# Performance work log

Hardware: AMD Instinct MI355X
Metric: run time of the kernel (lower is better)

The kernel has to match this reference:

```python
import jax, jax.numpy as jnp
import numpy as np

D = 10       # window length (days)
STRIDE = 10  # window stride


def setup_inputs() -> dict:
    key = jax.random.key(0)
    X = jax.random.normal(key, (16384, 15, 100), dtype=jnp.float32)
    return {"X": X}


def reference(X):
    # X: [B, n, T]
    B, n, T = X.shape
    w = (T - D) // STRIDE + 1
    # Gather all windows at once: [B, n, w, D]
    idx = jnp.arange(w)[:, None] * STRIDE + jnp.arange(D)[None, :]  # [w, D]
    win = X[:, :, idx]  # [B, n, w, D]

    mean = jnp.mean(win, axis=-1, keepdims=True)
    c = win - mean                                  # centered, [B, n, w, D]
    # torch.std is unbiased (ddof=1)
    std = jnp.sqrt(jnp.sum(c * c, axis=-1) / (D - 1))  # [B, n, w]

    # Population covariance between all channel pairs via one batched Gram matmul
    gram = jnp.einsum('biwd,bjwd->bijw', c, c) / D   # [B, n, n, w]

    # Pair order in the original: j=0..n-2 paired with k=j+1..n-1 == row-major upper triangle
    ii, jj = jnp.triu_indices(n, k=1)
    cov = gram[:, ii, jj]                            # [B, h, w]
    corr = cov / (std[:, ii] * std[:, jj])           # [B, h, w]
    return corr
```

## Files before the change

kernel.cpp:

```cpp
#include <hip/hip_runtime.h>


#define NB    16384
#define NSER  15
#define TLEN  100
#define DWIN  10
#define WCNT  10
#define NPAIR 105

__global__ __launch_bounds__(64, 3) void ts_corr_kernel(const float* __restrict__ X,
                                                        float* __restrict__ out) {
    const int task = blockIdx.x * 64 + threadIdx.x;
    const int b = task / WCNT;
    const int w = task % WCNT;

    const float* Xb = X + (size_t)b * (NSER * TLEN) + w * DWIN;

    float win[NSER][DWIN];
    #pragma unroll
    for (int i = 0; i < NSER; ++i) {
        const float2* p2 = reinterpret_cast<const float2*>(Xb + i * TLEN);
        #pragma unroll
        for (int k = 0; k < 5; ++k) {
            float2 v = p2[k];
            win[i][2 * k]     = v.x;
            win[i][2 * k + 1] = v.y;
        }
    }

    float istd[NSER];
    #pragma unroll
    for (int i = 0; i < NSER; ++i) {
        float s = 0.f;
        #pragma unroll
        for (int d = 0; d < DWIN; ++d) s += win[i][d];
        const float m = s * (1.0f / DWIN);
        float sq = 0.f;
        #pragma unroll
        for (int d = 0; d < DWIN; ++d) {
            const float c = win[i][d] - m;
            win[i][d] = c;
            sq += c * c;
        }
        istd[i] = rsqrtf(sq * (1.0f / (DWIN - 1)));
    }

    float* o = out + (size_t)b * (NPAIR * WCNT) + w;
    int p = 0;
    #pragma unroll
    for (int i = 0; i < NSER; ++i) {
        #pragma unroll
        for (int j = i + 1; j < NSER; ++j) {
            float dot = 0.f;
            #pragma unroll
            for (int d = 0; d < DWIN; ++d) dot += win[i][d] * win[j][d];
            o[(size_t)p * WCNT] = dot * (1.0f / DWIN) * istd[i] * istd[j];
            ++p;
        }
    }
}

extern "C" void kernel_launch(void* const* d_in, const int* in_sizes, int n_in,
                              void* d_out, int out_size, void* d_ws, size_t ws_size,
                              hipStream_t stream) {
    const float* X = (const float*)d_in[0];
    float* out = (float*)d_out;
    const int total = NB * WCNT;
    const int block = 64;
    const int grid = (total + block - 1) / block;
    ts_corr_kernel<<<grid, block, 0, stream>>>(X, out);
}
```

Measured before the change: 188.9 us.

## Stage tiles through LDS with async global_load_lds double buffering

Replaces the one-thread-per-window kernel with a persistent grid of 256 blocks. Each block double-buffers 8-batch input tiles into LDS using global_load_lds, computes correlations from LDS in register groups of 5 series using sum-of-squares statistics, stages the outputs in LDS, and writes them back with coalesced float4 stores. The aim is coalesced, overlapped memory traffic and fewer live registers. In exchange only 80 of 128 threads compute, the grid is small, and the one-pass variance formula is less numerically stable.

```diff
diff --git a/kernel.cpp b/kernel.cpp
--- a/kernel.cpp
+++ b/kernel.cpp
@@ -1,62 +1,144 @@
 #include <hip/hip_runtime.h>
+#include <stdint.h>
 
 
-#define NB    16384
-#define NSER  15
-#define TLEN  100
-#define DWIN  10
-#define WCNT  10
-#define NPAIR 105
+#define NSER   15
+#define TLEN   100
+#define DWIN   10
+#define WCNT   10
+#define NPAIR  105
+#define TB     8
+#define NTHR   128
+#define NBLK   256
+#define TPB    8
+#define IN_F   (TB * NSER * TLEN)
+#define OUT_F  (TB * NPAIR * WCNT)
+#define LDS_BYTES ((2 * IN_F + OUT_F) * 4)
 
-__global__ __launch_bounds__(64, 3) void ts_corr_kernel(const float* __restrict__ X,
-                                                        float* __restrict__ out) {
-    const int task = blockIdx.x * 64 + threadIdx.x;
-    const int b = task / WCNT;
-    const int w = task % WCNT;
-
-    const float* Xb = X + (size_t)b * (NSER * TLEN) + w * DWIN;
-
-    float win[NSER][DWIN];
+__device__ inline void issue_tile_copy(const float* __restrict__ g, float* l, int tid) {
     #pragma unroll
-    for (int i = 0; i < NSER; ++i) {
-        const float2* p2 = reinterpret_cast<const float2*>(Xb + i * TLEN);
-        #pragma unroll
-        for (int k = 0; k < 5; ++k) {
-            float2 v = p2[k];
-            win[i][2 * k]     = v.x;
-            win[i][2 * k + 1] = v.y;
+    for (int k0 = 0; k0 < 3000; k0 += NTHR) {
+        const int k = k0 + tid;
+        if (k < 3000) {
+            __builtin_amdgcn_global_load_lds(
+                (const __attribute__((address_space(1))) uint32_t*)(g + k * 4),
+                (__attribute__((address_space(3))) uint32_t*)(l + k * 4),
+                16, 0, 0);
         }
     }
+}
 
-    float istd[NSER];
+template <int G>
+__device__ inline void load_group(const float* base, float R[5][DWIN]) {
     #pragma unroll
-    for (int i = 0; i < NSER; ++i) {
-        float s = 0.f;
+    for (int r = 0; r < 5; ++r) {
         #pragma unroll
-        for (int d = 0; d < DWIN; ++d) s += win[i][d];
-        const float m = s * (1.0f / DWIN);
-        float sq = 0.f;
+        for (int d = 0; d < DWIN; d += 2) {
+            float2 v = *reinterpret_cast<const float2*>(base + (G * 5 + r) * TLEN + d);
+            R[r][d] = v.x; R[r][d + 1] = v.y;
+        }
+    }
+}
+
+template <int G>
+__device__ inline void stats(const float R[5][DWIN], float* mu, float* isd) {
+    #pragma unroll
+    for (int r = 0; r < 5; ++r) {
+        float s1 = 0.f, s2 = 0.f;
         #pragma unroll
-        for (int d = 0; d < DWIN; ++d) {
-            const float c = win[i][d] - m;
-            win[i][d] = c;
-            sq += c * c;
-        }
-        istd[i] = rsqrtf(sq * (1.0f / (DWIN - 1)));
+        for (int d = 0; d < DWIN; ++d) { s1 += R[r][d]; s2 += R[r][d] * R[r][d]; }
+        const float m = s1 * 0.1f;
+        mu[G * 5 + r]  = m;
+        isd[G * 5 + r] = rsqrtf((s2 - 10.f * m * m) * (1.f / 9.f));
     }
+}
 
-    float* o = out + (size_t)b * (NPAIR * WCNT) + w;
-    int p = 0;
+__device__ inline void emit(float* ob, int i, int j, float dot,
+                            const float* mu, const float* isd) {
+    const int p = i * (29 - i) / 2 + (j - i - 1);
+    ob[p * WCNT] = (dot * 0.1f - mu[i] * mu[j]) * isd[i] * isd[j];
+}
+
+template <int GA, int GB>
+__device__ inline void dots_rect(const float A[5][DWIN], const float B[5][DWIN],
+                                 const float* mu, const float* isd, float* ob) {
     #pragma unroll
-    for (int i = 0; i < NSER; ++i) {
+    for (int ri = 0; ri < 5; ++ri) {
         #pragma unroll
-        for (int j = i + 1; j < NSER; ++j) {
+        for (int rj = 0; rj < 5; ++rj) {
             float dot = 0.f;
             #pragma unroll
-            for (int d = 0; d < DWIN; ++d) dot += win[i][d] * win[j][d];
-            o[(size_t)p * WCNT] = dot * (1.0f / DWIN) * istd[i] * istd[j];
-            ++p;
+            for (int d = 0; d < DWIN; ++d) dot += A[ri][d] * B[rj][d];
+            emit(ob, GA * 5 + ri, GB * 5 + rj, dot, mu, isd);
         }
+    }
+}
+
+template <int G>
+__device__ inline void dots_tri(const float A[5][DWIN],
+                                const float* mu, const float* isd, float* ob) {
+    #pragma unroll
+    for (int ri = 0; ri < 5; ++ri) {
+        #pragma unroll
+        for (int rj = ri + 1; rj < 5; ++rj) {
+            float dot = 0.f;
+            #pragma unroll
+            for (int d = 0; d < DWIN; ++d) dot += A[ri][d] * A[rj][d];
+            emit(ob, G * 5 + ri, G * 5 + rj, dot, mu, isd);
+        }
+    }
+}
+
+__global__ __launch_bounds__(NTHR, 2) void ts_corr_kernel(const float* __restrict__ X,
+                                                          float* __restrict__ out) {
+    extern __shared__ float smem[];
+    float* in0   = smem;
+    float* in1   = smem + IN_F;
+    float* out_s = smem + 2 * IN_F;
+
+    const int tid = threadIdx.x;
+    const int blk = blockIdx.x;
+
+    issue_tile_copy(X + (size_t)(blk * TPB) * IN_F, in0, tid);
+    __syncthreads();
+
+    for (int t = 0; t < TPB; ++t) {
+        float* cur = (t & 1) ? in1 : in0;
+        float* nxt = (t & 1) ? in0 : in1;
+        const size_t tile = (size_t)(blk * TPB + t);
+
+        if (t + 1 < TPB)
+            issue_tile_copy(X + (tile + 1) * IN_F, nxt, tid);
+
+        if (tid < TB * WCNT) {
+            const int b_l = tid / WCNT, w = tid % WCNT;
+            const float* base = cur + b_l * (NSER * TLEN) + w * DWIN;
+            float* ob = out_s + b_l * (NPAIR * WCNT) + w;
+            float A[5][DWIN], B[5][DWIN], mu[NSER], isd[NSER];
+
+            load_group<0>(base, A); stats<0>(A, mu, isd);
+            dots_tri<0>(A, mu, isd, ob);
+            load_group<1>(base, B); stats<1>(B, mu, isd);
+            dots_rect<0, 1>(A, B, mu, isd, ob);
+            dots_tri<1>(B, mu, isd, ob);
+            load_group<2>(base, A); stats<2>(A, mu, isd);
+            dots_rect<1, 2>(B, A, mu, isd, ob);
+            dots_tri<2>(A, mu, isd, ob);
+            load_group<0>(base, B);
+            dots_rect<0, 2>(B, A, mu, isd, ob);
+        }
+        __syncthreads();
+
+        float* og = out + tile * OUT_F;
+        #pragma unroll
+        for (int k0 = 0; k0 < 2100; k0 += NTHR) {
+            const int k = k0 + tid;
+            if (k < 2100) {
+                float4 v = *reinterpret_cast<const float4*>(out_s + k * 4);
+                *reinterpret_cast<float4*>(og + k * 4) = v;
+            }
+        }
+        __syncthreads();
     }
 }
 
@@ -65,8 +147,7 @@
                               hipStream_t stream) {
     const float* X = (const float*)d_in[0];
     float* out = (float*)d_out;
-    const int total = NB * WCNT;
-    const int block = 64;
-    const int grid = (total + block - 1) / block;
-    ts_corr_kernel<<<grid, block, 0, stream>>>(X, out);
+    (void)hipFuncSetAttribute((const void*)ts_corr_kernel,
+                              hipFuncAttributeMaxDynamicSharedMemorySize, LDS_BYTES);
+    ts_corr_kernel<<<NBLK, NTHR, LDS_BYTES, stream>>>(X, out);
 }
```

Result: slower. 201.1 us (+6.4%).
